# Optimization experiments

Measured on AMD Instinct MI355X. Metric: run time of the kernel, lower is better.

## Reference

```python
import jax, jax.numpy as jnp
import numpy as np

KS = 3  # kernel_size
OUTC = 3
FEATC = 6
PATCH = FEATC * KS * KS  # 54


def setup_inputs() -> dict:
    key = jax.random.key(0)
    k1, k2 = jax.random.split(key)
    B, H, W = 4, 512, 512
    feat = jax.random.normal(k1, (B, FEATC, H, W), dtype=jnp.float32)
    kernel_map = jax.random.normal(k2, (B, OUTC * PATCH, H, W), dtype=jnp.float32)
    return {"feat": feat, "kernel_map": kernel_map}


def _extract_patches(feat):
    # feat: [B, C, H, W] -> [B, C*9, H, W] matching torch.nn.Unfold(3, padding=1)
    # channel ordering: c*9 + (ky*3 + kx)  (channel outermost, then kernel row, col)
    B, C, H, W = feat.shape
    pad = jnp.pad(feat, ((0, 0), (0, 0), (1, 1), (1, 1)))
    shifts = [pad[:, :, dy:dy + H, dx:dx + W] for dy in range(KS) for dx in range(KS)]
    patches = jnp.stack(shifts, axis=2)  # [B, C, 9, H, W]
    return patches.reshape(B, C * KS * KS, H, W)


def reference(feat, kernel_map):
    B, _, H, W = feat.shape
    patches = _extract_patches(feat)                      # [B, 54, H, W]
    km = kernel_map.reshape(B, OUTC, PATCH, H, W)         # [B, 3, 54, H, W]
    # per-pixel dot product: out[b,o,h,w] = sum_k patches[b,k,h,w] * km[b,o,k,h,w]
    out = jnp.einsum('bkhw,bokhw->bohw', patches, km)
    return out
```

## Files before the change

kernel.cpp:

```cpp
#include <hip/hip_runtime.h>

#define KS 3
#define OUTC 3
#define FEATC 6
#define PATCH (FEATC * KS * KS)

typedef float f32x4 __attribute__((ext_vector_type(4)));

__global__ __launch_bounds__(256) void supersample_kernel(
    const float* __restrict__ feat,
    const float* __restrict__ km,
    float* __restrict__ out,
    int B, int H, int W)
{
    const int Wq = W >> 2;
    const int total = B * OUTC * H * Wq;
    int idx = blockIdx.x * blockDim.x + threadIdx.x;
    if (idx >= total) return;

    const int wq = idx % Wq;
    int t = idx / Wq;
    const int h = t % H;  t /= H;
    const int o = t % OUTC;
    const int b = t / OUTC;
    const int w0 = wq << 2;

    const size_t HW = (size_t)H * (size_t)W;
    const float* featb = feat + (size_t)b * FEATC * HW;
    const float* kmo   = km   + ((size_t)b * OUTC + o) * PATCH * HW
                               + (size_t)h * W + w0;
    float*       outp  = out  + ((size_t)b * OUTC + o) * HW + (size_t)h * W + w0;

    f32x4 acc = (f32x4)0.f;

#pragma unroll
    for (int c = 0; c < FEATC; ++c) {
        float r[3][6];
#pragma unroll
        for (int ky = 0; ky < 3; ++ky) {
            const int hy = h + ky - 1;
            if (hy < 0 || hy >= H) {
#pragma unroll
                for (int j = 0; j < 6; ++j) r[ky][j] = 0.f;
            } else {
                const float* row = featb + (size_t)c * HW + (size_t)hy * W;
                const f32x4 mid = *reinterpret_cast<const f32x4*>(row + w0);
                r[ky][1] = mid.x; r[ky][2] = mid.y; r[ky][3] = mid.z; r[ky][4] = mid.w;
                r[ky][0] = (w0 > 0)     ? row[w0 - 1] : 0.f;
                r[ky][5] = (w0 + 4 < W) ? row[w0 + 4] : 0.f;
            }
        }

        const float* kmc = kmo + (size_t)(c * KS * KS) * HW;
        f32x4 k4[9];
#pragma unroll
        for (int t9 = 0; t9 < 9; ++t9) {
            k4[t9] = __builtin_nontemporal_load(
                reinterpret_cast<const f32x4*>(kmc + (size_t)t9 * HW));
        }
#pragma unroll
        for (int ky = 0; ky < 3; ++ky) {
#pragma unroll
            for (int kx = 0; kx < 3; ++kx) {
                const f32x4 k = k4[ky * 3 + kx];
                acc.x = fmaf(r[ky][kx + 0], k.x, acc.x);
                acc.y = fmaf(r[ky][kx + 1], k.y, acc.y);
                acc.z = fmaf(r[ky][kx + 2], k.z, acc.z);
                acc.w = fmaf(r[ky][kx + 3], k.w, acc.w);
            }
        }
    }

    *reinterpret_cast<f32x4*>(outp) = acc;
}

extern "C" void kernel_launch(void* const* d_in, const int* in_sizes, int n_in,
                              void* d_out, int out_size, void* d_ws, size_t ws_size,
                              hipStream_t stream) {
    const float* feat = (const float*)d_in[0];
    const float* km   = (const float*)d_in[1];
    float* out        = (float*)d_out;

    const int B = 4, H = 512, W = 512;
    const int total = B * OUTC * H * (W >> 2);
    const int block = 256;
    const int grid  = (total + block - 1) / block;
    supersample_kernel<<<grid, block, 0, stream>>>(feat, km, out, B, H, W);
}
```

Measured before the change: 145.9 us.

## Double-buffer kernel-map loads across channels and shuffle halo pixels

Kernel-map loads for the next feature channel are now issued before the current channel's FMAs, using two register buffers (ka/kb), so memory latency overlaps with compute. The left and right halo values for each row now come from neighbouring lanes through warp shuffles, and only the edge lanes of each 64-wide wavefront fall back to scalar global loads. This trades higher register pressure, which may lower occupancy, for fewer scalar loads and more loads in flight. The kernel is dominated by streaming the large kernel map from memory, so the gain may be limited.

```diff
diff --git a/kernel.cpp b/kernel.cpp
--- a/kernel.cpp
+++ b/kernel.cpp
@@ -15,8 +15,9 @@
 {
     const int Wq = W >> 2;
     const int total = B * OUTC * H * Wq;
-    int idx = blockIdx.x * blockDim.x + threadIdx.x;
+    const int idx = blockIdx.x * blockDim.x + threadIdx.x;
     if (idx >= total) return;
+    const int lane = threadIdx.x & 63;
 
     const int wq = idx % Wq;
     int t = idx / Wq;
@@ -32,44 +33,62 @@
     float*       outp  = out  + ((size_t)b * OUTC + o) * HW + (size_t)h * W + w0;
 
     f32x4 acc = (f32x4)0.f;
+    f32x4 ka[9], kb[9];
 
 #pragma unroll
-    for (int c = 0; c < FEATC; ++c) {
-        float r[3][6];
-#pragma unroll
-        for (int ky = 0; ky < 3; ++ky) {
-            const int hy = h + ky - 1;
-            if (hy < 0 || hy >= H) {
-#pragma unroll
-                for (int j = 0; j < 6; ++j) r[ky][j] = 0.f;
-            } else {
-                const float* row = featb + (size_t)c * HW + (size_t)hy * W;
-                const f32x4 mid = *reinterpret_cast<const f32x4*>(row + w0);
-                r[ky][1] = mid.x; r[ky][2] = mid.y; r[ky][3] = mid.z; r[ky][4] = mid.w;
-                r[ky][0] = (w0 > 0)     ? row[w0 - 1] : 0.f;
-                r[ky][5] = (w0 + 4 < W) ? row[w0 + 4] : 0.f;
-            }
-        }
+    for (int t9 = 0; t9 < 9; ++t9)
+        ka[t9] = __builtin_nontemporal_load(
+            reinterpret_cast<const f32x4*>(kmo + (size_t)t9 * HW));
 
-        const float* kmc = kmo + (size_t)(c * KS * KS) * HW;
-        f32x4 k4[9];
-#pragma unroll
-        for (int t9 = 0; t9 < 9; ++t9) {
-            k4[t9] = __builtin_nontemporal_load(
-                reinterpret_cast<const f32x4*>(kmc + (size_t)t9 * HW));
-        }
-#pragma unroll
-        for (int ky = 0; ky < 3; ++ky) {
-#pragma unroll
-            for (int kx = 0; kx < 3; ++kx) {
-                const f32x4 k = k4[ky * 3 + kx];
-                acc.x = fmaf(r[ky][kx + 0], k.x, acc.x);
-                acc.y = fmaf(r[ky][kx + 1], k.y, acc.y);
-                acc.z = fmaf(r[ky][kx + 2], k.z, acc.z);
-                acc.w = fmaf(r[ky][kx + 3], k.w, acc.w);
-            }
-        }
+#define STEP(c, CUR, NXT)                                                      \
+    {                                                                          \
+        if ((c) + 1 < FEATC) {                                                 \
+            const float* kmn = kmo + (size_t)(((c) + 1) * 9) * HW;             \
+            _Pragma("unroll")                                                  \
+            for (int t9 = 0; t9 < 9; ++t9)                                     \
+                NXT[t9] = __builtin_nontemporal_load(                          \
+                    reinterpret_cast<const f32x4*>(kmn + (size_t)t9 * HW));    \
+        }                                                                      \
+        float r[3][6];                                                         \
+        _Pragma("unroll")                                                      \
+        for (int ky = 0; ky < 3; ++ky) {                                       \
+            const int hy = h + ky - 1;                                         \
+            if (hy < 0 || hy >= H) {                                           \
+                _Pragma("unroll")                                              \
+                for (int j = 0; j < 6; ++j) r[ky][j] = 0.f;                    \
+            } else {                                                           \
+                const float* row = featb + (size_t)(c) * HW + (size_t)hy * W;  \
+                const f32x4 mid = *reinterpret_cast<const f32x4*>(row + w0);   \
+                float left  = __shfl_up(mid.w, 1);                             \
+                float right = __shfl_down(mid.x, 1);                           \
+                if (lane == 0)  left  = (w0 > 0)     ? row[w0 - 1] : 0.f;      \
+                if (lane == 63) right = (w0 + 4 < W) ? row[w0 + 4] : 0.f;      \
+                r[ky][0] = left;                                               \
+                r[ky][1] = mid.x; r[ky][2] = mid.y;                            \
+                r[ky][3] = mid.z; r[ky][4] = mid.w;                            \
+                r[ky][5] = right;                                              \
+            }                                                                  \
+        }                                                                      \
+        _Pragma("unroll")                                                      \
+        for (int ky = 0; ky < 3; ++ky) {                                       \
+            _Pragma("unroll")                                                  \
+            for (int kx = 0; kx < 3; ++kx) {                                   \
+                const f32x4 k = CUR[ky * 3 + kx];                              \
+                acc.x = fmaf(r[ky][kx + 0], k.x, acc.x);                       \
+                acc.y = fmaf(r[ky][kx + 1], k.y, acc.y);                       \
+                acc.z = fmaf(r[ky][kx + 2], k.z, acc.z);                       \
+                acc.w = fmaf(r[ky][kx + 3], k.w, acc.w);                       \
+            }                                                                  \
+        }                                                                      \
     }
+
+    STEP(0, ka, kb)
+    STEP(1, kb, ka)
+    STEP(2, ka, kb)
+    STEP(3, kb, ka)
+    STEP(4, ka, kb)
+    STEP(5, kb, ka)
+#undef STEP
 
     *reinterpret_cast<f32x4*>(outp) = acc;
 }
```

New measurement: 155.0 us. 1.06x slower.
